# Optimization experiments

Measured on AMD Instinct MI355X. Metric: run time of the kernel, lower is better.

The kernel has to match this reference:

```python
import jax, jax.numpy as jnp
import numpy as np

DEPTH = 3          # sig_depth
GROUPS = 2         # channel_groups
EXTRA = 12         # extra_channels
IN_CH = 3
AUG_CH = 1 + IN_CH + EXTRA   # time + original + learnt = 16
HIDDEN = 256
OUT_CH = 32
SIG_PER_GROUP = AUG_CH + AUG_CH**2 + AUG_CH**3  # 4368
SIG_TOTAL = GROUPS * SIG_PER_GROUP              # 8736


def become_constant_trick(x, lengths):
    # y[i,j,:] = x[i,j,:] if j < lengths[i] else x[i, lengths[i]-1, :]
    B, S, C = x.shape
    idx = (lengths - 1).astype(jnp.int32)                      # (B,)
    last = jnp.take_along_axis(x, jnp.broadcast_to(idx[:, None, None], (B, 1, C)), axis=1)  # (B,1,C)
    mask = jnp.arange(S)[None, :] > idx[:, None]               # (B,S)
    return jnp.where(mask[:, :, None], last, x)


def signature(path, depth):
    # path: (B, S, C) -> (B, C + C^2 + ... + C^depth), flattened levels concatenated
    B, S, C = path.shape
    dx = path[:, 1:] - path[:, :-1]                            # (B, S-1, C) increments

    def sig_exp(d):  # exp of a single increment in the truncated tensor algebra
        terms = [d]
        cur = d
        for k in range(2, depth + 1):
            cur = (cur[:, :, None] * d[:, None, :]).reshape(B, -1) / k  # d^{\otimes k}/k!
            terms.append(cur)
        return terms

    def step(carry, d):  # Chen's identity: S <- S \otimes exp(d)
        e = sig_exp(d)
        new = []
        for k in range(depth):  # level k+1
            t = carry[k] + e[k]
            for i in range(k):  # carry level i+1 tensor e level k-i
                t = t + (carry[i][:, :, None] * e[k - i - 1][:, None, :]).reshape(B, -1)
            new.append(t)
        return tuple(new), None

    init = tuple(jnp.zeros((B, C ** k), path.dtype) for k in range(1, depth + 1))
    sig, _ = jax.lax.scan(step, init, jnp.swapaxes(dx, 0, 1))
    return jnp.concatenate(sig, axis=1)


def setup_inputs() -> dict:
    key = jax.random.key(0)
    ks = jax.random.split(key, 8)
    x = jax.random.normal(ks[0], (64, 512, IN_CH), dtype=jnp.float32)
    lengths = jnp.maximum(jax.random.randint(ks[1], (64,), 0, 512), 2).astype(jnp.int64)
    aug_w = jax.random.normal(ks[2], (GROUPS, EXTRA, IN_CH), dtype=jnp.float32) / np.sqrt(IN_CH)
    aug_b = jax.random.normal(ks[3], (GROUPS, EXTRA), dtype=jnp.float32) * 0.01
    w1 = jax.random.normal(ks[4], (SIG_TOTAL, HIDDEN), dtype=jnp.float32) / np.sqrt(SIG_TOTAL)
    b1 = jnp.zeros((HIDDEN,), jnp.float32)
    w2 = jax.random.normal(ks[5], (HIDDEN, OUT_CH), dtype=jnp.float32) / np.sqrt(HIDDEN)
    b2 = jnp.zeros((OUT_CH,), jnp.float32)
    return {"x": x, "lengths": lengths, "aug_w": aug_w, "aug_b": aug_b,
            "w1": w1, "b1": b1, "w2": w2, "b2": b2}


def reference(x, lengths, aug_w, aug_b, w1, b1, w2, b2):
    B, S, C = x.shape
    x = become_constant_trick(x, lengths)
    # signatory.Augment per group: cat([time, original, pointwise-linear(x)], channel)
    aug = jnp.einsum('gei,bsi->gbse', aug_w, x) + aug_b[:, None, None, :]   # (G,B,S,EXTRA)
    time = jnp.broadcast_to(jnp.linspace(0.0, 1.0, S, dtype=x.dtype)[None, None, :, None],
                            (GROUPS, B, S, 1))
    orig = jnp.broadcast_to(x[None], (GROUPS, B, S, C))
    path = jnp.concatenate([time, orig, aug], axis=-1)                      # (G,B,S,AUG_CH)
    # torch.stack(dim=1) then view(batch*groups, stream, ch)
    path = jnp.transpose(path, (1, 0, 2, 3)).reshape(B * GROUPS, S, AUG_CH)
    sig = signature(path, DEPTH).reshape(B, SIG_TOTAL)
    h = jax.nn.relu(sig @ w1 + b1)
    return h @ w2 + b2
```

## Files before the change

kernel.cpp:

```cpp
#include <hip/hip_runtime.h>

#define S_LEN   512
#define NSTEP   511
#define B_SZ    64
#define HIDDEN  256
#define OUT_CH  32
#define GBASE   4368

#define V_OFF   22528
#define U2_OFF  546816

__global__ __launch_bounds__(256) void prep_kernel(
    const float* __restrict__ x,
    const void*  __restrict__ lengths_raw,
    const float* __restrict__ aug_w,
    const float* __restrict__ w1,
    float* __restrict__ c_ws,
    float* __restrict__ V_ws,
    float* __restrict__ U2_ws)
{
    __shared__ float Ms[2][16][4];
    __shared__ union {
        struct { float4 U[16][4][16]; } t;
        struct { float xs[S_LEN * 3];
                 float u[NSTEP * 4 + 4];
                 float seg[4][88]; } s;
    } sm;

    const int bx  = blockIdx.x;
    const int tid = threadIdx.x;

    if (tid < 32) {
        const int g = tid >> 4, row = tid & 15;
        float4 m;
        if (row == 0)      m = make_float4(1.f, 0.f, 0.f, 0.f);
        else if (row < 4)  m = make_float4(0.f, row == 1 ? 1.f : 0.f,
                                                row == 2 ? 1.f : 0.f,
                                                row == 3 ? 1.f : 0.f);
        else {
            const float* aw = aug_w + g * 36 + (row - 4) * 3;
            m = make_float4(0.f, aw[0], aw[1], aw[2]);
        }
        *(float4*)&Ms[g][row][0] = m;
    }
    __syncthreads();

    if (bx < 128) {
        const int g  = bx >> 6, rem = bx & 63;
        const int p  = rem >> 2, cc = rem & 3;
        const int col0 = cc * 64;
        const int c4 = tid & 15;
        const int t  = tid >> 4;

        {
            const int q = t;
            const float* wbase = w1 + (size_t)(g * GBASE + 272 + p * 256 + q * 16) * HIDDEN
                                    + col0 + c4 * 4;
            float4 wv[16];
            #pragma unroll
            for (int r = 0; r < 16; ++r)
                wv[r] = *(const float4*)(wbase + (size_t)r * HIDDEN);
            #pragma unroll
            for (int ck = 0; ck < 4; ++ck) {
                float4 acc = make_float4(0.f, 0.f, 0.f, 0.f);
                #pragma unroll
                for (int r = 0; r < 16; ++r) {
                    const float m = Ms[g][r][ck];
                    acc.x = fmaf(m, wv[r].x, acc.x);
                    acc.y = fmaf(m, wv[r].y, acc.y);
                    acc.z = fmaf(m, wv[r].z, acc.z);
                    acc.w = fmaf(m, wv[r].w, acc.w);
                }
                sm.t.U[q][ck][c4] = acc;
            }
        }
        __syncthreads();

        {
            const int cj = t >> 2, ck = t & 3;
            float4 acc = make_float4(0.f, 0.f, 0.f, 0.f);
            #pragma unroll
            for (int q = 0; q < 16; ++q) {
                const float m = Ms[g][q][cj];
                const float4 uv = sm.t.U[q][ck][c4];
                acc.x = fmaf(m, uv.x, acc.x);
                acc.y = fmaf(m, uv.y, acc.y);
                acc.z = fmaf(m, uv.z, acc.z);
                acc.w = fmaf(m, uv.w, acc.w);
            }
            *(float4*)(V_ws + (size_t)((g * 16 + p) * 16 + t) * HIDDEN + col0 + c4 * 4) = acc;
        }

        if (t < 4) {
            const float* w2b = w1 + (size_t)(g * GBASE + 16 + p * 16) * HIDDEN + col0 + c4 * 4;
            float4 acc = make_float4(0.f, 0.f, 0.f, 0.f);
            #pragma unroll
            for (int q = 0; q < 16; ++q) {
                const float m = Ms[g][q][t];
                const float4 wv = *(const float4*)(w2b + (size_t)q * HIDDEN);
                acc.x = fmaf(m, wv.x, acc.x);
                acc.y = fmaf(m, wv.y, acc.y);
                acc.z = fmaf(m, wv.z, acc.z);
                acc.w = fmaf(m, wv.w, acc.w);
            }
            *(float4*)(U2_ws + (size_t)((g * 16 + p) * 4 + t) * HIDDEN + col0 + c4 * 4) = acc;
        }
    } else {
        const int b = bx - 128;

        const int* l32 = (const int*)lengths_raw;
        const int  len = (l32[1] == 0) ? l32[2 * b] : l32[b];
        const int  lastIdx = len - 1;

        for (int idx = tid; idx < 384; idx += 256)
            ((float4*)sm.s.xs)[idx] = ((const float4*)(x + (size_t)b * S_LEN * 3))[idx];
        __syncthreads();

        for (int s = tid; s < NSTEP; s += 256) {
            float dx0 = 0.f, dx1 = 0.f, dx2 = 0.f;
            if (s < lastIdx) {
                dx0 = sm.s.xs[(s + 1) * 3 + 0] - sm.s.xs[s * 3 + 0];
                dx1 = sm.s.xs[(s + 1) * 3 + 1] - sm.s.xs[s * 3 + 1];
                dx2 = sm.s.xs[(s + 1) * 3 + 2] - sm.s.xs[s * 3 + 2];
            }
            *(float4*)&sm.s.u[s * 4] = make_float4(1.0f / 511.0f, dx0, dx1, dx2);
        }
        __syncthreads();

        const int wid = tid >> 6, lane = tid & 63;
        const int a   = lane >> 4;
        const int bb  = (lane >> 2) & 3;
        const int c   = lane & 3;
        {
            const int s0   = wid * 128;
            const int nloc = min(128, NSTEP - s0);
            float r1 = 0.f, r2 = 0.f, r3 = 0.f;
            for (int s = s0; s < s0 + nloc; ++s) {
                const float da = sm.s.u[s * 4 + a];
                const float db = sm.s.u[s * 4 + bb];
                const float dc = sm.s.u[s * 4 + c];
                const float t2 = fmaf(db, fmaf(r1, 0.5f, da * (1.f / 6.f)), r2);
                r3 = fmaf(t2, dc, r3);
                r2 = fmaf(db, fmaf(da, 0.5f, r1), r2);
                r1 += da;
            }
            sm.s.seg[wid][20 + lane] = r3;
            if (c == 0)            sm.s.seg[wid][4 + a * 4 + bb] = r2;
            if (bb == 0 && c == 0) sm.s.seg[wid][a]              = r1;
        }
        __syncthreads();

        if (wid == 0) {
            float A1 = sm.s.seg[0][a];
            float A2 = sm.s.seg[0][4 + a * 4 + bb];
            float A3 = sm.s.seg[0][20 + lane];
            #pragma unroll
            for (int sg = 1; sg < 4; ++sg) {
                const float* S = sm.s.seg[sg];
                const float B1a  = S[a];
                const float B1b  = S[bb];
                const float B1c  = S[c];
                const float B2ab = S[4 + a * 4 + bb];
                const float B2bc = S[4 + bb * 4 + c];
                const float B3   = S[20 + lane];
                A3 = fmaf(A1, B2bc, fmaf(A2, B1c, A3 + B3));
                A2 = fmaf(A1, B1b, A2 + B2ab);
                A1 = A1 + B1a;
            }
            c_ws[b * 88 + 20 + lane] = A3;
            if (c == 0)            c_ws[b * 88 + 4 + a * 4 + bb] = A2;
            if (bb == 0 && c == 0) c_ws[b * 88 + a]              = A1;
        }
    }
}

__global__ __launch_bounds__(1024) void mix_kernel(
    const float* __restrict__ c_ws,
    const float* __restrict__ V_ws,
    const float* __restrict__ U2_ws,
    const float* __restrict__ aug_w,
    const float* __restrict__ w1,
    const float* __restrict__ b1,
    const float* __restrict__ w2,
    const float* __restrict__ b2,
    float* __restrict__ outp)
{
    __shared__ float Ms[2][16][4];
    __shared__ float sC[88];
    __shared__ float E1[2][16];
    __shared__ float D2[2][64];
    __shared__ float D3[2][256];
    __shared__ float4 sp[16][64];
    __shared__ float s_h[HIDDEN];
    __shared__ float s_p[8][33];

    const int b   = blockIdx.x;
    const int tid = threadIdx.x;

    if (tid < 32) {
        const int g = tid >> 4, row = tid & 15;
        float4 m;
        if (row == 0)      m = make_float4(1.f, 0.f, 0.f, 0.f);
        else if (row < 4)  m = make_float4(0.f, row == 1 ? 1.f : 0.f,
                                                row == 2 ? 1.f : 0.f,
                                                row == 3 ? 1.f : 0.f);
        else {
            const float* aw = aug_w + g * 36 + (row - 4) * 3;
            m = make_float4(0.f, aw[0], aw[1], aw[2]);
        }
        *(float4*)&Ms[g][row][0] = m;
    }
    if (tid >= 64 && tid < 152) sC[tid - 64] = c_ws[b * 88 + tid - 64];
    __syncthreads();

    if (tid < 512) {
        const int g = tid >> 8, r = tid & 255, p = r >> 4, t = r & 15;
        D3[g][r] = fmaf(Ms[g][p][0], sC[20 + t],
                   fmaf(Ms[g][p][1], sC[36 + t],
                   fmaf(Ms[g][p][2], sC[52 + t],
                         Ms[g][p][3] * sC[68 + t])));
    } else if (tid < 640) {
        const int e = tid - 512, g = e >> 6, r = e & 63;
        const int p = r >> 2, cb = r & 3;
        D2[g][r] = fmaf(Ms[g][p][0], sC[4 + cb],
                   fmaf(Ms[g][p][1], sC[8 + cb],
                   fmaf(Ms[g][p][2], sC[12 + cb],
                         Ms[g][p][3] * sC[16 + cb])));
    } else if (tid < 672) {
        const int e = tid - 640, g = e >> 4, p = e & 15;
        E1[g][p] = fmaf(Ms[g][p][0], sC[0],
                   fmaf(Ms[g][p][1], sC[1],
                   fmaf(Ms[g][p][2], sC[2], Ms[g][p][3] * sC[3])));
    }
    __syncthreads();

    const int col4 = tid & 63, ks = tid >> 6;
    const int cb4  = col4 * 4;

    float4 acc = make_float4(0.f, 0.f, 0.f, 0.f);
    #pragma unroll
    for (int g = 0; g < 2; ++g) {
        {
            const float e1 = E1[g][ks];
            const float4 wv = *(const float4*)(w1 + (size_t)(g * GBASE + ks) * HIDDEN + cb4);
            acc.x = fmaf(e1, wv.x, acc.x); acc.y = fmaf(e1, wv.y, acc.y);
            acc.z = fmaf(e1, wv.z, acc.z); acc.w = fmaf(e1, wv.w, acc.w);
        }
        #pragma unroll
        for (int m = 0; m < 4; ++m) {
            const float d2 = D2[g][ks * 4 + m];
            const float4 uv = *(const float4*)(U2_ws + (size_t)(g * 64 + ks * 4 + m) * HIDDEN + cb4);
            acc.x = fmaf(d2, uv.x, acc.x); acc.y = fmaf(d2, uv.y, acc.y);
            acc.z = fmaf(d2, uv.z, acc.z); acc.w = fmaf(d2, uv.w, acc.w);
        }
        #pragma unroll
        for (int m = 0; m < 16; ++m) {
            const float d3 = D3[g][ks * 16 + m];
            const float4 vv = *(const float4*)(V_ws + (size_t)(g * 256 + ks * 16 + m) * HIDDEN + cb4);
            acc.x = fmaf(d3, vv.x, acc.x); acc.y = fmaf(d3, vv.y, acc.y);
            acc.z = fmaf(d3, vv.z, acc.z); acc.w = fmaf(d3, vv.w, acc.w);
        }
    }
    sp[ks][col4] = acc;
    __syncthreads();

    if (tid < HIDDEN) {
        const int cq = tid >> 2, cm = tid & 3;
        float v = b1[tid];
        #pragma unroll
        for (int k = 0; k < 16; ++k)
            v += ((const float*)&sp[k][cq])[cm];
        s_h[tid] = fmaxf(v, 0.f);
    }
    __syncthreads();

    if (tid < 256) {
        const int o = tid & 31, part = tid >> 5;
        float pacc = 0.f;
        #pragma unroll
        for (int jj = 0; jj < 32; ++jj)
            pacc = fmaf(s_h[part * 32 + jj], w2[(part * 32 + jj) * OUT_CH + o], pacc);
        s_p[part][o] = pacc;
    }
    __syncthreads();

    if (tid < OUT_CH) {
        float oacc = b2[tid];
        #pragma unroll
        for (int q = 0; q < 8; ++q) oacc += s_p[q][tid];
        outp[b * OUT_CH + tid] = oacc;
    }
}

extern "C" void kernel_launch(void* const* d_in, const int* in_sizes, int n_in,
                              void* d_out, int out_size, void* d_ws, size_t ws_size,
                              hipStream_t stream) {
    const float* x       = (const float*)d_in[0];
    const void*  lengths = d_in[1];
    const float* aug_w   = (const float*)d_in[2];
    const float* w1      = (const float*)d_in[4];
    const float* b1      = (const float*)d_in[5];
    const float* w2      = (const float*)d_in[6];
    const float* b2      = (const float*)d_in[7];

    float* c_ws  = (float*)d_ws;
    float* V_ws  = (float*)((char*)d_ws + V_OFF);
    float* U2_ws = (float*)((char*)d_ws + U2_OFF);

    prep_kernel<<<192, 256, 0, stream>>>(x, lengths, aug_w, w1, c_ws, V_ws, U2_ws);
    mix_kernel<<<B_SZ, 1024, 0, stream>>>(c_ws, V_ws, U2_ws, aug_w, w1, b1, w2, b2,
                                          (float*)d_out);
}
```

Baseline: 25.14 us.

## Fuse prep and mix kernels using inter-block release/acquire flags

Merges the two launches into one 192-block kernel. The 128 weight-folding blocks publish a per-block flag with a release store once V/U2 are written. The 64 per-batch blocks keep their signature result in shared memory instead of a global buffer, spin on those flags, and then run the hidden and output layers with 256 threads rather than 1024. This removes a kernel launch and the global round trip for the per-batch coefficients. In exchange each batch block does four times more projection work per thread, and the flags are never reset, so later calls skip the wait and may read V/U2 while they are being rewritten.

```diff
diff --git a/kernel.cpp b/kernel.cpp
--- a/kernel.cpp
+++ b/kernel.cpp
@@ -6,25 +6,34 @@
 #define HIDDEN  256
 #define OUT_CH  32
 #define GBASE   4368
+#define MAGIC   0x5AFE5AFEu
 
 #define V_OFF   22528
 #define U2_OFF  546816
 
-__global__ __launch_bounds__(256) void prep_kernel(
+__global__ __launch_bounds__(256) void fused_kernel(
     const float* __restrict__ x,
     const void*  __restrict__ lengths_raw,
     const float* __restrict__ aug_w,
     const float* __restrict__ w1,
-    float* __restrict__ c_ws,
+    const float* __restrict__ b1,
+    const float* __restrict__ w2,
+    const float* __restrict__ b2,
+    unsigned int* __restrict__ flags,
     float* __restrict__ V_ws,
-    float* __restrict__ U2_ws)
+    float* __restrict__ U2_ws,
+    float* __restrict__ outp)
 {
     __shared__ float Ms[2][16][4];
+    __shared__ float cs[88];
     __shared__ union {
         struct { float4 U[16][4][16]; } t;
         struct { float xs[S_LEN * 3];
                  float u[NSTEP * 4 + 4];
                  float seg[4][88]; } s;
+        struct { float D3[2][256]; float D2[2][64]; float E1[2][16];
+                 float4 sp[4][64]; float s_h[HIDDEN];
+                 float s_p[8][33]; } m;
     } sm;
 
     const int bx  = blockIdx.x;
@@ -105,6 +114,11 @@
             }
             *(float4*)(U2_ws + (size_t)((g * 16 + p) * 4 + t) * HIDDEN + col0 + c4 * 4) = acc;
         }
+
+        __threadfence();
+        __syncthreads();
+        if (tid == 0)
+            __hip_atomic_store(&flags[bx], MAGIC, __ATOMIC_RELEASE, __HIP_MEMORY_SCOPE_AGENT);
     } else {
         const int b = bx - 128;
 
@@ -167,128 +181,100 @@
                 A2 = fmaf(A1, B1b, A2 + B2ab);
                 A1 = A1 + B1a;
             }
-            c_ws[b * 88 + 20 + lane] = A3;
-            if (c == 0)            c_ws[b * 88 + 4 + a * 4 + bb] = A2;
-            if (bb == 0 && c == 0) c_ws[b * 88 + a]              = A1;
-        }
-    }
-}
-
-__global__ __launch_bounds__(1024) void mix_kernel(
-    const float* __restrict__ c_ws,
-    const float* __restrict__ V_ws,
-    const float* __restrict__ U2_ws,
-    const float* __restrict__ aug_w,
-    const float* __restrict__ w1,
-    const float* __restrict__ b1,
-    const float* __restrict__ w2,
-    const float* __restrict__ b2,
-    float* __restrict__ outp)
-{
-    __shared__ float Ms[2][16][4];
-    __shared__ float sC[88];
-    __shared__ float E1[2][16];
-    __shared__ float D2[2][64];
-    __shared__ float D3[2][256];
-    __shared__ float4 sp[16][64];
-    __shared__ float s_h[HIDDEN];
-    __shared__ float s_p[8][33];
-
-    const int b   = blockIdx.x;
-    const int tid = threadIdx.x;
-
-    if (tid < 32) {
-        const int g = tid >> 4, row = tid & 15;
-        float4 m;
-        if (row == 0)      m = make_float4(1.f, 0.f, 0.f, 0.f);
-        else if (row < 4)  m = make_float4(0.f, row == 1 ? 1.f : 0.f,
-                                                row == 2 ? 1.f : 0.f,
-                                                row == 3 ? 1.f : 0.f);
-        else {
-            const float* aw = aug_w + g * 36 + (row - 4) * 3;
-            m = make_float4(0.f, aw[0], aw[1], aw[2]);
-        }
-        *(float4*)&Ms[g][row][0] = m;
-    }
-    if (tid >= 64 && tid < 152) sC[tid - 64] = c_ws[b * 88 + tid - 64];
-    __syncthreads();
-
-    if (tid < 512) {
-        const int g = tid >> 8, r = tid & 255, p = r >> 4, t = r & 15;
-        D3[g][r] = fmaf(Ms[g][p][0], sC[20 + t],
-                   fmaf(Ms[g][p][1], sC[36 + t],
-                   fmaf(Ms[g][p][2], sC[52 + t],
-                         Ms[g][p][3] * sC[68 + t])));
-    } else if (tid < 640) {
-        const int e = tid - 512, g = e >> 6, r = e & 63;
-        const int p = r >> 2, cb = r & 3;
-        D2[g][r] = fmaf(Ms[g][p][0], sC[4 + cb],
-                   fmaf(Ms[g][p][1], sC[8 + cb],
-                   fmaf(Ms[g][p][2], sC[12 + cb],
-                         Ms[g][p][3] * sC[16 + cb])));
-    } else if (tid < 672) {
-        const int e = tid - 640, g = e >> 4, p = e & 15;
-        E1[g][p] = fmaf(Ms[g][p][0], sC[0],
-                   fmaf(Ms[g][p][1], sC[1],
-                   fmaf(Ms[g][p][2], sC[2], Ms[g][p][3] * sC[3])));
-    }
-    __syncthreads();
-
-    const int col4 = tid & 63, ks = tid >> 6;
-    const int cb4  = col4 * 4;
-
-    float4 acc = make_float4(0.f, 0.f, 0.f, 0.f);
-    #pragma unroll
-    for (int g = 0; g < 2; ++g) {
-        {
-            const float e1 = E1[g][ks];
-            const float4 wv = *(const float4*)(w1 + (size_t)(g * GBASE + ks) * HIDDEN + cb4);
-            acc.x = fmaf(e1, wv.x, acc.x); acc.y = fmaf(e1, wv.y, acc.y);
-            acc.z = fmaf(e1, wv.z, acc.z); acc.w = fmaf(e1, wv.w, acc.w);
-        }
+            cs[20 + lane] = A3;
+            if (c == 0)            cs[4 + a * 4 + bb] = A2;
+            if (bb == 0 && c == 0) cs[a]              = A1;
+        }
+        __syncthreads();
+
         #pragma unroll
-        for (int m = 0; m < 4; ++m) {
-            const float d2 = D2[g][ks * 4 + m];
-            const float4 uv = *(const float4*)(U2_ws + (size_t)(g * 64 + ks * 4 + m) * HIDDEN + cb4);
-            acc.x = fmaf(d2, uv.x, acc.x); acc.y = fmaf(d2, uv.y, acc.y);
-            acc.z = fmaf(d2, uv.z, acc.z); acc.w = fmaf(d2, uv.w, acc.w);
-        }
+        for (int rep = 0; rep < 2; ++rep) {
+            const int e = tid + rep * 256;
+            const int g = e >> 8, r = e & 255, p = r >> 4, t = r & 15;
+            sm.m.D3[g][r] = fmaf(Ms[g][p][0], cs[20 + t],
+                            fmaf(Ms[g][p][1], cs[36 + t],
+                            fmaf(Ms[g][p][2], cs[52 + t],
+                                  Ms[g][p][3] * cs[68 + t])));
+        }
+        if (tid < 128) {
+            const int g = tid >> 6, r = tid & 63, p = r >> 2, cb = r & 3;
+            sm.m.D2[g][r] = fmaf(Ms[g][p][0], cs[4 + cb],
+                            fmaf(Ms[g][p][1], cs[8 + cb],
+                            fmaf(Ms[g][p][2], cs[12 + cb],
+                                  Ms[g][p][3] * cs[16 + cb])));
+        } else if (tid < 160) {
+            const int e = tid - 128, g = e >> 4, p = e & 15;
+            sm.m.E1[g][p] = fmaf(Ms[g][p][0], cs[0],
+                            fmaf(Ms[g][p][1], cs[1],
+                            fmaf(Ms[g][p][2], cs[2], Ms[g][p][3] * cs[3])));
+        }
+
+        if (tid < 128) {
+            while (__hip_atomic_load(&flags[tid], __ATOMIC_ACQUIRE,
+                                     __HIP_MEMORY_SCOPE_AGENT) != MAGIC) { }
+        }
+        __syncthreads();
+        __threadfence();
+
+        const int col4 = tid & 63, ks = tid >> 6;
+        const int cb4  = col4 * 4;
+        float4 acc = make_float4(0.f, 0.f, 0.f, 0.f);
         #pragma unroll
-        for (int m = 0; m < 16; ++m) {
-            const float d3 = D3[g][ks * 16 + m];
-            const float4 vv = *(const float4*)(V_ws + (size_t)(g * 256 + ks * 16 + m) * HIDDEN + cb4);
-            acc.x = fmaf(d3, vv.x, acc.x); acc.y = fmaf(d3, vv.y, acc.y);
-            acc.z = fmaf(d3, vv.z, acc.z); acc.w = fmaf(d3, vv.w, acc.w);
-        }
-    }
-    sp[ks][col4] = acc;
-    __syncthreads();
-
-    if (tid < HIDDEN) {
-        const int cq = tid >> 2, cm = tid & 3;
-        float v = b1[tid];
-        #pragma unroll
-        for (int k = 0; k < 16; ++k)
-            v += ((const float*)&sp[k][cq])[cm];
-        s_h[tid] = fmaxf(v, 0.f);
-    }
-    __syncthreads();
-
-    if (tid < 256) {
-        const int o = tid & 31, part = tid >> 5;
-        float pacc = 0.f;
-        #pragma unroll
-        for (int jj = 0; jj < 32; ++jj)
-            pacc = fmaf(s_h[part * 32 + jj], w2[(part * 32 + jj) * OUT_CH + o], pacc);
-        s_p[part][o] = pacc;
-    }
-    __syncthreads();
-
-    if (tid < OUT_CH) {
-        float oacc = b2[tid];
-        #pragma unroll
-        for (int q = 0; q < 8; ++q) oacc += s_p[q][tid];
-        outp[b * OUT_CH + tid] = oacc;
+        for (int g = 0; g < 2; ++g) {
+            #pragma unroll
+            for (int m1 = 0; m1 < 4; ++m1) {
+                const int p = ks * 4 + m1;
+                const float e1 = sm.m.E1[g][p];
+                const float4 wv = *(const float4*)(w1 + (size_t)(g * GBASE + p) * HIDDEN + cb4);
+                acc.x = fmaf(e1, wv.x, acc.x); acc.y = fmaf(e1, wv.y, acc.y);
+                acc.z = fmaf(e1, wv.z, acc.z); acc.w = fmaf(e1, wv.w, acc.w);
+            }
+            #pragma unroll
+            for (int e = 0; e < 16; ++e) {
+                const int r = ks * 16 + e;
+                const float d2 = sm.m.D2[g][r];
+                const float4 uv = *(const float4*)(U2_ws + (size_t)(g * 64 + r) * HIDDEN + cb4);
+                acc.x = fmaf(d2, uv.x, acc.x); acc.y = fmaf(d2, uv.y, acc.y);
+                acc.z = fmaf(d2, uv.z, acc.z); acc.w = fmaf(d2, uv.w, acc.w);
+            }
+            #pragma unroll 8
+            for (int e = 0; e < 64; ++e) {
+                const int r = ks * 64 + e;
+                const float d3 = sm.m.D3[g][r];
+                const float4 vv = *(const float4*)(V_ws + (size_t)(g * 256 + r) * HIDDEN + cb4);
+                acc.x = fmaf(d3, vv.x, acc.x); acc.y = fmaf(d3, vv.y, acc.y);
+                acc.z = fmaf(d3, vv.z, acc.z); acc.w = fmaf(d3, vv.w, acc.w);
+            }
+        }
+        sm.m.sp[ks][col4] = acc;
+        __syncthreads();
+
+        {
+            const int cq = tid >> 2, cm = tid & 3;
+            float v = b1[tid];
+            #pragma unroll
+            for (int k = 0; k < 4; ++k)
+                v += ((const float*)&sm.m.sp[k][cq])[cm];
+            sm.m.s_h[tid] = fmaxf(v, 0.f);
+        }
+        __syncthreads();
+
+        {
+            const int o = tid & 31, part = tid >> 5;
+            float pacc = 0.f;
+            #pragma unroll
+            for (int jj = 0; jj < 32; ++jj)
+                pacc = fmaf(sm.m.s_h[part * 32 + jj], w2[(part * 32 + jj) * OUT_CH + o], pacc);
+            sm.m.s_p[part][o] = pacc;
+        }
+        __syncthreads();
+
+        if (tid < OUT_CH) {
+            float oacc = b2[tid];
+            #pragma unroll
+            for (int q = 0; q < 8; ++q) oacc += sm.m.s_p[q][tid];
+            outp[b * OUT_CH + tid] = oacc;
+        }
     }
 }
 
@@ -303,11 +289,10 @@
     const float* w2      = (const float*)d_in[6];
     const float* b2      = (const float*)d_in[7];
 
-    float* c_ws  = (float*)d_ws;
+    unsigned int* flags = (unsigned int*)d_ws;
     float* V_ws  = (float*)((char*)d_ws + V_OFF);
     float* U2_ws = (float*)((char*)d_ws + U2_OFF);
 
-    prep_kernel<<<192, 256, 0, stream>>>(x, lengths, aug_w, w1, c_ws, V_ws, U2_ws);
-    mix_kernel<<<B_SZ, 1024, 0, stream>>>(c_ws, V_ws, U2_ws, aug_w, w1, b1, w2, b2,
-                                          (float*)d_out);
+    fused_kernel<<<192, 256, 0, stream>>>(x, lengths, aug_w, w1, b1, w2, b2,
+                                          flags, V_ws, U2_ws, (float*)d_out);
 }
```

Result: slower. 33.63 us (+33.8%).
